# Kernel tuning notes

Measured on AMD Instinct MI355X. Metric: run time of the kernel, lower is better.

The kernel has to match this reference:

```python
import jax, jax.numpy as jnp
import numpy as np

NEG_SLOPE = 0.2  # PyG GATConv default
EPS = 1e-16      # PyG softmax denominator epsilon


def gat_layer(x, W, a_src, a_dst, b, src, dst, num_nodes, concat):
    """One PyG-style GATConv layer (eval mode, self-loops already in src/dst)."""
    H, F = a_src.shape
    h = (x @ W).reshape(num_nodes, H, F)                      # [N,H,F]
    alpha_src = jnp.einsum('nhf,hf->nh', h, a_src)            # [N,H]
    alpha_dst = jnp.einsum('nhf,hf->nh', h, a_dst)            # [N,H]
    e = jax.nn.leaky_relu(alpha_src[src] + alpha_dst[dst], NEG_SLOPE)  # [E,H]
    # segment softmax over incoming edges of each dst node
    emax = jax.ops.segment_max(e, dst, num_segments=num_nodes)
    emax = jnp.where(jnp.isfinite(emax), emax, 0.0)
    ex = jnp.exp(e - emax[dst])
    denom = jax.ops.segment_sum(ex, dst, num_segments=num_nodes)
    alpha = ex / (denom[dst] + EPS)                           # [E,H]
    out = jax.ops.segment_sum(alpha[:, :, None] * h[src], dst,
                              num_segments=num_nodes)         # [N,H,F]
    out = out.reshape(num_nodes, H * F) if concat else out.mean(axis=1)
    return out + b


def setup_inputs() -> dict:
    key = jax.random.key(0)
    ks = jax.random.split(key, 12)
    N, E, IN, HID, HEADS = 50000, 800000, 64, 32, 2
    x = jax.random.normal(ks[0], (N, IN), dtype=jnp.float32)
    edge_index = jax.random.randint(ks[1], (2, E), 0, N, dtype=jnp.int64)
    s = 0.1
    # layer 1: in_dim -> hidden per head, heads=2, concat
    W1 = jax.random.normal(ks[2], (IN, HEADS * HID), dtype=jnp.float32) * s
    a_src1 = jax.random.normal(ks[3], (HEADS, HID), dtype=jnp.float32) * s
    a_dst1 = jax.random.normal(ks[4], (HEADS, HID), dtype=jnp.float32) * s
    b1 = jax.random.normal(ks[5], (HEADS * HID,), dtype=jnp.float32) * s
    # layer 2: hidden*heads -> hidden, heads=1
    W2 = jax.random.normal(ks[6], (HEADS * HID, HID), dtype=jnp.float32) * s
    a_src2 = jax.random.normal(ks[7], (1, HID), dtype=jnp.float32) * s
    a_dst2 = jax.random.normal(ks[8], (1, HID), dtype=jnp.float32) * s
    b2 = jax.random.normal(ks[9], (HID,), dtype=jnp.float32) * s
    return {"x": x, "edge_index": edge_index, "W1": W1, "a_src1": a_src1,
            "a_dst1": a_dst1, "b1": b1, "W2": W2, "a_src2": a_src2,
            "a_dst2": a_dst2, "b2": b2}


def reference(x, edge_index, W1, a_src1, a_dst1, b1, W2, a_src2, a_dst2, b2):
    N = x.shape[0]
    loop = jnp.arange(N, dtype=edge_index.dtype)
    src = jnp.concatenate([edge_index[0], loop])  # add_self_loops=True
    dst = jnp.concatenate([edge_index[1], loop])
    h = jax.nn.relu(gat_layer(x, W1, a_src1, a_dst1, b1, src, dst, N, True))
    return gat_layer(h, W2, a_src2, a_dst2, b2, src, dst, N, True)
```

## Files before the change

### kernel.cpp

```cpp
#include <hip/hip_runtime.h>
#include <hip/hip_fp16.h>

#define TPB 256
#define NEG_SLOPE 0.2f
#define B1 256
#define DPB 512
#define MAXNB 128

__device__ __forceinline__ int getIdx(const void* p, int is32, long long i) {
  return is32 ? ((const int*)p)[i] : (int)((const long long*)p)[i];
}

__global__ __launch_bounds__(TPB) void k_histA(
    const void* __restrict__ ei, int E, int Etot,
    int* __restrict__ histA, int NB, int CH) {
  __shared__ int lh[MAXNB];
  __shared__ int sflag;
  int b = blockIdx.x, tid = threadIdx.x;
  for (int i = tid; i < NB; i += TPB) lh[i] = 0;
  if (tid < 64) {
    const unsigned long long* p = (const unsigned long long*)ei;
    unsigned long long m = __ballot(tid < E && p[tid] > 0xFFFFFFFFULL);
    if (tid == 0) sflag = (m != 0ULL) ? 1 : 0;
  }
  __syncthreads();
  int f = sflag;
  int beg = b * CH, end = min(beg + CH, Etot);
  for (int e = beg + tid; e < end; e += TPB) {
    int d = (e < E) ? getIdx(ei, f, (long long)E + e) : e - E;
    atomicAdd(&lh[d / DPB], 1);
  }
  __syncthreads();
  for (int i = tid; i < NB; i += TPB) histA[b * NB + i] = lh[i];
}

__global__ __launch_bounds__(TPB) void k_placeB(
    const void* __restrict__ ei, int E, int Etot,
    const int* __restrict__ histA, int* __restrict__ bucketBase,
    int2* __restrict__ pairs, int NB, int CH) {
  __shared__ int cur[MAXNB];
  __shared__ int sh[TPB];
  __shared__ int sflag;
  int b = blockIdx.x, tid = threadIdx.x;
  int before = 0, tot = 0;
  if (tid < NB) {
    for (int bb = 0; bb < B1; ++bb) {
      int v = histA[bb * NB + tid];
      tot += v;
      if (bb < b) before += v;
    }
  }
  if (tid < 64) {
    const unsigned long long* p = (const unsigned long long*)ei;
    unsigned long long m = __ballot(tid < E && p[tid] > 0xFFFFFFFFULL);
    if (tid == 0) sflag = (m != 0ULL) ? 1 : 0;
  }
  sh[tid] = (tid < NB) ? tot : 0;
  __syncthreads();
  for (int off = 1; off < TPB; off <<= 1) {
    int v = (tid >= off) ? sh[tid - off] : 0;
    __syncthreads();
    sh[tid] += v;
    __syncthreads();
  }
  int excl = sh[tid] - ((tid < NB) ? tot : 0);
  if (tid < NB) cur[tid] = excl + before;
  if (b == 0 && tid < NB) bucketBase[tid] = excl;
  if (b == 0 && tid == NB - 1) bucketBase[NB] = sh[tid];
  int f = sflag;
  __syncthreads();
  int beg = b * CH, end = min(beg + CH, Etot);
  for (int e = beg + tid; e < end; e += TPB) {
    int s, d;
    if (e < E) {
      s = getIdx(ei, f, e);
      d = getIdx(ei, f, (long long)E + e);
    } else {
      s = d = e - E;
    }
    int pos = atomicAdd(&cur[d / DPB], 1);
    pairs[pos] = make_int2(s, d);
  }
}

__global__ __launch_bounds__(DPB) void k_bucket(
    const int2* __restrict__ pairs, const int* __restrict__ bucketBase,
    int* __restrict__ rowptr, int* __restrict__ csr_src, int N, int Etot) {
  __shared__ int cnt[DPB];
  __shared__ int sc[DPB];
  int g = blockIdx.x, tid = threadIdx.x;
  int base = g * DPB;
  int nd = N - base; if (nd > DPB) nd = DPB;
  cnt[tid] = 0;
  __syncthreads();
  int beg = bucketBase[g], end = bucketBase[g + 1];
  for (int j = beg + tid; j < end; j += DPB)
    atomicAdd(&cnt[pairs[j].y & (DPB - 1)], 1);
  __syncthreads();
  sc[tid] = cnt[tid];
  __syncthreads();
  for (int off = 1; off < DPB; off <<= 1) {
    int v = (tid >= off) ? sc[tid - off] : 0;
    __syncthreads();
    sc[tid] += v;
    __syncthreads();
  }
  int excl = beg + sc[tid] - cnt[tid];
  if (tid < nd) rowptr[base + tid] = excl;
  if (g == 0 && tid == 0) rowptr[N] = Etot;
  __syncthreads();
  cnt[tid] = excl;
  __syncthreads();
  for (int j = beg + tid; j < end; j += DPB) {
    int2 p = pairs[j];
    int pos = atomicAdd(&cnt[p.y & (DPB - 1)], 1);
    csr_src[pos] = p.x;
  }
}

__global__ __launch_bounds__(TPB) void k_gemm1(
    const float* __restrict__ x, const float* __restrict__ W1,
    const float* __restrict__ aS, const float* __restrict__ aD,
    __half* __restrict__ h1, float* __restrict__ asrc, float* __restrict__ adst, int N) {
  __shared__ float Wl[64 * 64];
  __shared__ float xr[4][64];
  int t = threadIdx.x;
  for (int i = t; i < 64 * 64; i += TPB) Wl[i] = W1[i];
  int w = t >> 6, lane = t & 63;
  int node = blockIdx.x * 4 + w;
  if (node < N) xr[w][lane] = x[(size_t)node * 64 + lane];
  __syncthreads();
  if (node >= N) return;
  float acc = 0.f;
#pragma unroll
  for (int k = 0; k < 64; ++k) acc = fmaf(xr[w][k], Wl[k * 64 + lane], acc);
  h1[(size_t)node * 64 + lane] = __float2half(acc);
  float vs = acc * aS[lane];
  float vd = acc * aD[lane];
#pragma unroll
  for (int m = 16; m >= 1; m >>= 1) {
    vs += __shfl_xor(vs, m, 64);
    vd += __shfl_xor(vd, m, 64);
  }
  if ((lane & 31) == 0) {
    asrc[node * 2 + (lane >> 5)] = vs;
    adst[node * 2 + (lane >> 5)] = vd;
  }
}

__global__ __launch_bounds__(TPB) void k_gather1f(
    const int* __restrict__ rowptr, const int* __restrict__ csr_src,
    const float* __restrict__ as1, const float* __restrict__ ad1,
    const __half* __restrict__ h1, const float* __restrict__ b1,
    const float* __restrict__ W2, const float* __restrict__ aS2,
    const float* __restrict__ aD2,
    __half* __restrict__ h2, float* __restrict__ as2, float* __restrict__ ad2, int N) {
  __shared__ float W2s[64 * 32];
  __shared__ float aS2s[32], aD2s[32];
  __shared__ int   sSid[8][32];
  __shared__ float sWp[8][64];
  __shared__ float rowBuf[8][64];
  int t = threadIdx.x;
  for (int i = t; i < 64 * 32; i += TPB) W2s[i] = W2[i];
  if (t < 32) { aS2s[t] = aS2[t]; aD2s[t] = aD2[t]; }
  __syncthreads();

  int hw = t >> 5, lane32 = t & 31;
  int node = blockIdx.x * 8 + hw;
  if (node >= N) return;

  int e4 = lane32 >> 3, c8 = lane32 & 7;
  int head = c8 >> 2;
  float2 adv = *(const float2*)(ad1 + (size_t)node * 2);
  int beg = rowptr[node], end = rowptr[node + 1];
  float a0 = 0.f, a1 = 0.f, a2 = 0.f, a3 = 0.f;
  float a4 = 0.f, a5 = 0.f, a6 = 0.f, a7 = 0.f;
  float d0L = 0.f, d1L = 0.f;
  for (int chunk = beg; chunk < end; chunk += 32) {
    int m = end - chunk; if (m > 32) m = 32;
    int sid = 0; float w0 = 0.f, w1 = 0.f;
    if (lane32 < m) {
      sid = csr_src[chunk + lane32];
      float2 av = *(const float2*)(as1 + (size_t)sid * 2);
      float v0 = av.x + adv.x, v1 = av.y + adv.y;
      v0 = v0 > 0.f ? v0 : NEG_SLOPE * v0;
      v1 = v1 > 0.f ? v1 : NEG_SLOPE * v1;
      w0 = __expf(v0); w1 = __expf(v1);
      d0L += w0; d1L += w1;
    }
    sSid[hw][lane32] = sid;
    *(float2*)&sWp[hw][lane32 * 2] = make_float2(w0, w1);
    for (int j = 0; j < m; j += 8) {
      int j0 = j + e4, j1 = j0 + 4;
      int s0 = sSid[hw][j0], s1 = sSid[hw][j1];
      float q0 = sWp[hw][j0 * 2 + head], q1 = sWp[hw][j1 * 2 + head];
      float4 r0 = *(const float4*)(h1 + (size_t)s0 * 64 + c8 * 8);
      float4 r1 = *(const float4*)(h1 + (size_t)s1 * 64 + c8 * 8);
      const __half2* p0 = (const __half2*)&r0;
      const __half2* p1 = (const __half2*)&r1;
      float2 u;
      u = __half22float2(p0[0]); a0 = fmaf(q0, u.x, a0); a1 = fmaf(q0, u.y, a1);
      u = __half22float2(p0[1]); a2 = fmaf(q0, u.x, a2); a3 = fmaf(q0, u.y, a3);
      u = __half22float2(p0[2]); a4 = fmaf(q0, u.x, a4); a5 = fmaf(q0, u.y, a5);
      u = __half22float2(p0[3]); a6 = fmaf(q0, u.x, a6); a7 = fmaf(q0, u.y, a7);
      u = __half22float2(p1[0]); a0 = fmaf(q1, u.x, a0); a1 = fmaf(q1, u.y, a1);
      u = __half22float2(p1[1]); a2 = fmaf(q1, u.x, a2); a3 = fmaf(q1, u.y, a3);
      u = __half22float2(p1[2]); a4 = fmaf(q1, u.x, a4); a5 = fmaf(q1, u.y, a5);
      u = __half22float2(p1[3]); a6 = fmaf(q1, u.x, a6); a7 = fmaf(q1, u.y, a7);
    }
  }
#pragma unroll
  for (int m2 = 8; m2 <= 16; m2 <<= 1) {
    a0 += __shfl_xor(a0, m2, 64); a1 += __shfl_xor(a1, m2, 64);
    a2 += __shfl_xor(a2, m2, 64); a3 += __shfl_xor(a3, m2, 64);
    a4 += __shfl_xor(a4, m2, 64); a5 += __shfl_xor(a5, m2, 64);
    a6 += __shfl_xor(a6, m2, 64); a7 += __shfl_xor(a7, m2, 64);
  }
#pragma unroll
  for (int m2 = 1; m2 <= 16; m2 <<= 1) {
    d0L += __shfl_xor(d0L, m2, 64);
    d1L += __shfl_xor(d1L, m2, 64);
  }
  float inv = 1.f / ((head == 0 ? d0L : d1L) + 1e-16f);
  if (e4 == 0) {
    float4 bb0 = *(const float4*)(b1 + c8 * 8);
    float4 bb1 = *(const float4*)(b1 + c8 * 8 + 4);
    float4 o0, o1;
    o0.x = fmaf(a0, inv, bb0.x); o0.y = fmaf(a1, inv, bb0.y);
    o0.z = fmaf(a2, inv, bb0.z); o0.w = fmaf(a3, inv, bb0.w);
    o1.x = fmaf(a4, inv, bb1.x); o1.y = fmaf(a5, inv, bb1.y);
    o1.z = fmaf(a6, inv, bb1.z); o1.w = fmaf(a7, inv, bb1.w);
    o0.x = o0.x > 0.f ? o0.x : 0.f; o0.y = o0.y > 0.f ? o0.y : 0.f;
    o0.z = o0.z > 0.f ? o0.z : 0.f; o0.w = o0.w > 0.f ? o0.w : 0.f;
    o1.x = o1.x > 0.f ? o1.x : 0.f; o1.y = o1.y > 0.f ? o1.y : 0.f;
    o1.z = o1.z > 0.f ? o1.z : 0.f; o1.w = o1.w > 0.f ? o1.w : 0.f;
    *(float4*)&rowBuf[hw][c8 * 8] = o0;
    *(float4*)&rowBuf[hw][c8 * 8 + 4] = o1;
  }
  int c = lane32;
  float acc2 = 0.f;
#pragma unroll
  for (int k = 0; k < 64; ++k)
    acc2 = fmaf(rowBuf[hw][k], W2s[k * 32 + c], acc2);
  h2[(size_t)node * 32 + c] = __float2half(acc2);
  float vs = acc2 * aS2s[c];
  float vd = acc2 * aD2s[c];
#pragma unroll
  for (int m2 = 1; m2 <= 16; m2 <<= 1) {
    vs += __shfl_xor(vs, m2, 64);
    vd += __shfl_xor(vd, m2, 64);
  }
  if (lane32 == 0) {
    as2[node] = vs;
    ad2[node] = vd;
  }
}

__global__ __launch_bounds__(TPB) void k_gather2(
    const int* __restrict__ rowptr, const int* __restrict__ csr_src,
    const float* __restrict__ as2, const float* __restrict__ ad2,
    const __half* __restrict__ h2, const float* __restrict__ b,
    float* __restrict__ out, int N) {
  __shared__ int   sS[8][32];
  __shared__ float sWv[8][32];
  int t = threadIdx.x;
  int hw = t >> 5, lane32 = t & 31;
  int wid = blockIdx.x * 8 + hw;
  if (wid >= N) return;
  int e8 = lane32 >> 2, c4 = lane32 & 3;
  float ad = ad2[wid];
  int beg = rowptr[wid], end = rowptr[wid + 1];
  float a0 = 0.f, a1 = 0.f, a2 = 0.f, a3 = 0.f;
  float a4 = 0.f, a5 = 0.f, a6 = 0.f, a7 = 0.f;
  float dL = 0.f;
  for (int chunk = beg; chunk < end; chunk += 32) {
    int m = end - chunk; if (m > 32) m = 32;
    int sid = 0; float wv = 0.f;
    if (lane32 < m) {
      sid = csr_src[chunk + lane32];
      float v = as2[sid] + ad;
      v = v > 0.f ? v : NEG_SLOPE * v;
      wv = __expf(v);
      dL += wv;
    }
    sS[hw][lane32] = sid;
    sWv[hw][lane32] = wv;
    for (int j = 0; j < m; j += 16) {
      int j0 = j + e8, j1 = j0 + 8;
      int s0 = sS[hw][j0], s1 = sS[hw][j1];
      float q0 = sWv[hw][j0], q1 = sWv[hw][j1];
      float4 r0 = *(const float4*)(h2 + (size_t)s0 * 32 + c4 * 8);
      float4 r1 = *(const float4*)(h2 + (size_t)s1 * 32 + c4 * 8);
      const __half2* p0 = (const __half2*)&r0;
      const __half2* p1 = (const __half2*)&r1;
      float2 u;
      u = __half22float2(p0[0]); a0 = fmaf(q0, u.x, a0); a1 = fmaf(q0, u.y, a1);
      u = __half22float2(p0[1]); a2 = fmaf(q0, u.x, a2); a3 = fmaf(q0, u.y, a3);
      u = __half22float2(p0[2]); a4 = fmaf(q0, u.x, a4); a5 = fmaf(q0, u.y, a5);
      u = __half22float2(p0[3]); a6 = fmaf(q0, u.x, a6); a7 = fmaf(q0, u.y, a7);
      u = __half22float2(p1[0]); a0 = fmaf(q1, u.x, a0); a1 = fmaf(q1, u.y, a1);
      u = __half22float2(p1[1]); a2 = fmaf(q1, u.x, a2); a3 = fmaf(q1, u.y, a3);
      u = __half22float2(p1[2]); a4 = fmaf(q1, u.x, a4); a5 = fmaf(q1, u.y, a5);
      u = __half22float2(p1[3]); a6 = fmaf(q1, u.x, a6); a7 = fmaf(q1, u.y, a7);
    }
  }
#pragma unroll
  for (int m2 = 4; m2 <= 16; m2 <<= 1) {
    a0 += __shfl_xor(a0, m2, 64); a1 += __shfl_xor(a1, m2, 64);
    a2 += __shfl_xor(a2, m2, 64); a3 += __shfl_xor(a3, m2, 64);
    a4 += __shfl_xor(a4, m2, 64); a5 += __shfl_xor(a5, m2, 64);
    a6 += __shfl_xor(a6, m2, 64); a7 += __shfl_xor(a7, m2, 64);
  }
#pragma unroll
  for (int m2 = 1; m2 <= 16; m2 <<= 1) dL += __shfl_xor(dL, m2, 64);
  if (e8 == 0) {
    float inv = 1.f / (dL + 1e-16f);
    float4 bv0 = *(const float4*)(b + c4 * 8);
    float4 bv1 = *(const float4*)(b + c4 * 8 + 4);
    float4 o0, o1;
    o0.x = fmaf(a0, inv, bv0.x); o0.y = fmaf(a1, inv, bv0.y);
    o0.z = fmaf(a2, inv, bv0.z); o0.w = fmaf(a3, inv, bv0.w);
    o1.x = fmaf(a4, inv, bv1.x); o1.y = fmaf(a5, inv, bv1.y);
    o1.z = fmaf(a6, inv, bv1.z); o1.w = fmaf(a7, inv, bv1.w);
    *(float4*)(out + (size_t)wid * 32 + c4 * 8) = o0;
    *(float4*)(out + (size_t)wid * 32 + c4 * 8 + 4) = o1;
  }
}

extern "C" void kernel_launch(void* const* d_in, const int* in_sizes, int n_in,
                              void* d_out, int out_size, void* d_ws, size_t ws_size,
                              hipStream_t stream) {
  const float* x   = (const float*)d_in[0];
  const void*  ei  = d_in[1];
  const float* W1  = (const float*)d_in[2];
  const float* aS1 = (const float*)d_in[3];
  const float* aD1 = (const float*)d_in[4];
  const float* b1  = (const float*)d_in[5];
  const float* W2  = (const float*)d_in[6];
  const float* aS2 = (const float*)d_in[7];
  const float* aD2 = (const float*)d_in[8];
  const float* b2  = (const float*)d_in[9];
  float* out = (float*)d_out;

  int N = in_sizes[0] / 64;
  int E = in_sizes[1] / 2;
  int Etot = E + N;
  int NB = (N + DPB - 1) / DPB;
  int CH = (Etot + B1 - 1) / B1;

  float* W = (float*)d_ws;
  size_t o = 0;
  __half* h1 = (__half*)(W + o); o += (size_t)N * 32;
  size_t regB = (size_t)(2 * (size_t)Etot > (size_t)N * 16 ? 2 * (size_t)Etot : (size_t)N * 16);
  int2* pairs = (int2*)(W + o);
  __half* h2  = (__half*)(W + o);
  o += regB;
  float* as1  = W + o; o += (size_t)N * 2;
  float* ad1  = W + o; o += (size_t)N * 2;
  float* as2  = W + o; o += (size_t)N;
  float* ad2  = W + o; o += (size_t)N;
  int* ip = (int*)(W + o);
  size_t io = 0;
  int* histA      = ip + io; io += (size_t)NB * B1;
  int* bucketBase = ip + io; io += NB + 1;
  int* rowptr     = ip + io; io += N + 1;
  int* csr_src    = ip + io; io += Etot;

  k_histA<<<B1, TPB, 0, stream>>>(ei, E, Etot, histA, NB, CH);
  k_placeB<<<B1, TPB, 0, stream>>>(ei, E, Etot, histA, bucketBase, pairs, NB, CH);
  k_bucket<<<NB, DPB, 0, stream>>>(pairs, bucketBase, rowptr, csr_src, N, Etot);

  k_gemm1<<<(N + 3) / 4, TPB, 0, stream>>>(x, W1, aS1, aD1, h1, as1, ad1, N);
  k_gather1f<<<(N + 7) / 8, TPB, 0, stream>>>(rowptr, csr_src, as1, ad1, h1, b1,
                                              W2, aS2, aD2, h2, as2, ad2, N);

  k_gather2<<<(N + 7) / 8, TPB, 0, stream>>>(rowptr, csr_src, as2, ad2, h2, b2, out, N);
}
```

Measured before the change: 125.6 us.

## Co-schedule layer-1 GEMM blocks inside CSR histogram and placement kernels

```diff
diff --git a/kernel.cpp b/kernel.cpp
--- a/kernel.cpp
+++ b/kernel.cpp
@@ -11,11 +11,51 @@
   return is32 ? ((const int*)p)[i] : (int)((const long long*)p)[i];
 }
 
-__global__ __launch_bounds__(TPB) void k_histA(
+
+__device__ __forceinline__ void gemm1_body(
+    int gb, const float* __restrict__ x, const float* __restrict__ W1,
+    const float* __restrict__ aS, const float* __restrict__ aD,
+    __half* __restrict__ h1, float* __restrict__ asrc, float* __restrict__ adst,
+    int N, float* Wl, float (*xr)[64]) {
+  int t = threadIdx.x;
+  for (int i = t; i < 64 * 64; i += TPB) Wl[i] = W1[i];
+  int w = t >> 6, lane = t & 63;
+  int node = gb * 4 + w;
+  if (node < N) xr[w][lane] = x[(size_t)node * 64 + lane];
+  __syncthreads();
+  if (node >= N) return;
+  float acc = 0.f;
+#pragma unroll
+  for (int k = 0; k < 64; ++k) acc = fmaf(xr[w][k], Wl[k * 64 + lane], acc);
+  h1[(size_t)node * 64 + lane] = __float2half(acc);
+  float vs = acc * aS[lane];
+  float vd = acc * aD[lane];
+#pragma unroll
+  for (int m = 16; m >= 1; m >>= 1) {
+    vs += __shfl_xor(vs, m, 64);
+    vd += __shfl_xor(vd, m, 64);
+  }
+  if ((lane & 31) == 0) {
+    asrc[node * 2 + (lane >> 5)] = vs;
+    adst[node * 2 + (lane >> 5)] = vd;
+  }
+}
+
+__global__ __launch_bounds__(TPB) void k_fat1(
     const void* __restrict__ ei, int E, int Etot,
-    int* __restrict__ histA, int NB, int CH) {
+    int* __restrict__ histA, int NB, int CH,
+    const float* __restrict__ x, const float* __restrict__ W1,
+    const float* __restrict__ aS, const float* __restrict__ aD,
+    __half* __restrict__ h1, float* __restrict__ asrc, float* __restrict__ adst,
+    int N) {
+  __shared__ float Wl[64 * 64];
+  __shared__ float xr[4][64];
   __shared__ int lh[MAXNB];
   __shared__ int sflag;
+  if (blockIdx.x >= B1) {
+    gemm1_body((int)blockIdx.x - B1, x, W1, aS, aD, h1, asrc, adst, N, Wl, xr);
+    return;
+  }
   int b = blockIdx.x, tid = threadIdx.x;
   for (int i = tid; i < NB; i += TPB) lh[i] = 0;
   if (tid < 64) {
@@ -34,13 +74,23 @@
   for (int i = tid; i < NB; i += TPB) histA[b * NB + i] = lh[i];
 }
 
-__global__ __launch_bounds__(TPB) void k_placeB(
+__global__ __launch_bounds__(TPB) void k_fat2(
     const void* __restrict__ ei, int E, int Etot,
     const int* __restrict__ histA, int* __restrict__ bucketBase,
-    int2* __restrict__ pairs, int NB, int CH) {
+    int2* __restrict__ pairs, int NB, int CH,
+    const float* __restrict__ x, const float* __restrict__ W1,
+    const float* __restrict__ aS, const float* __restrict__ aD,
+    __half* __restrict__ h1, float* __restrict__ asrc, float* __restrict__ adst,
+    int N, int gOff) {
+  __shared__ float Wl[64 * 64];
+  __shared__ float xr[4][64];
   __shared__ int cur[MAXNB];
   __shared__ int sh[TPB];
   __shared__ int sflag;
+  if (blockIdx.x >= B1) {
+    gemm1_body((int)blockIdx.x - B1 + gOff, x, W1, aS, aD, h1, asrc, adst, N, Wl, xr);
+    return;
+  }
   int b = blockIdx.x, tid = threadIdx.x;
   int before = 0, tot = 0;
   if (tid < NB) {
@@ -115,36 +165,6 @@
     int2 p = pairs[j];
     int pos = atomicAdd(&cnt[p.y & (DPB - 1)], 1);
     csr_src[pos] = p.x;
-  }
-}
-
-__global__ __launch_bounds__(TPB) void k_gemm1(
-    const float* __restrict__ x, const float* __restrict__ W1,
-    const float* __restrict__ aS, const float* __restrict__ aD,
-    __half* __restrict__ h1, float* __restrict__ asrc, float* __restrict__ adst, int N) {
-  __shared__ float Wl[64 * 64];
-  __shared__ float xr[4][64];
-  int t = threadIdx.x;
-  for (int i = t; i < 64 * 64; i += TPB) Wl[i] = W1[i];
-  int w = t >> 6, lane = t & 63;
-  int node = blockIdx.x * 4 + w;
-  if (node < N) xr[w][lane] = x[(size_t)node * 64 + lane];
-  __syncthreads();
-  if (node >= N) return;
-  float acc = 0.f;
-#pragma unroll
-  for (int k = 0; k < 64; ++k) acc = fmaf(xr[w][k], Wl[k * 64 + lane], acc);
-  h1[(size_t)node * 64 + lane] = __float2half(acc);
-  float vs = acc * aS[lane];
-  float vd = acc * aD[lane];
-#pragma unroll
-  for (int m = 16; m >= 1; m >>= 1) {
-    vs += __shfl_xor(vs, m, 64);
-    vd += __shfl_xor(vd, m, 64);
-  }
-  if ((lane & 31) == 0) {
-    asrc[node * 2 + (lane >> 5)] = vs;
-    adst[node * 2 + (lane >> 5)] = vd;
   }
 }
 
@@ -347,6 +367,8 @@
   int Etot = E + N;
   int NB = (N + DPB - 1) / DPB;
   int CH = (Etot + B1 - 1) / B1;
+  int gAll = (N + 3) / 4;
+  int g1 = gAll / 2, g2 = gAll - g1;
 
   float* W = (float*)d_ws;
   size_t o = 0;
@@ -366,11 +388,12 @@
   int* rowptr     = ip + io; io += N + 1;
   int* csr_src    = ip + io; io += Etot;
 
-  k_histA<<<B1, TPB, 0, stream>>>(ei, E, Etot, histA, NB, CH);
-  k_placeB<<<B1, TPB, 0, stream>>>(ei, E, Etot, histA, bucketBase, pairs, NB, CH);
+  k_fat1<<<B1 + g1, TPB, 0, stream>>>(ei, E, Etot, histA, NB, CH,
+                                      x, W1, aS1, aD1, h1, as1, ad1, N);
+  k_fat2<<<B1 + g2, TPB, 0, stream>>>(ei, E, Etot, histA, bucketBase, pairs, NB, CH,
+                                      x, W1, aS1, aD1, h1, as1, ad1, N, g1);
   k_bucket<<<NB, DPB, 0, stream>>>(pairs, bucketBase, rowptr, csr_src, N, Etot);
 
-  k_gemm1<<<(N + 3) / 4, TPB, 0, stream>>>(x, W1, aS1, aD1, h1, as1, ad1, N);
   k_gather1f<<<(N + 7) / 8, TPB, 0, stream>>>(rowptr, csr_src, as1, ad1, h1, b1,
                                               W2, aS2, aD2, h2, as2, ad2, N);
 
```

Result: faster. 106.9 us (-14.9%).
